# Kernel tuning notes

Hardware: AMD Instinct MI355X
Metric: run time of the kernel (lower is better)

Reference implementation:

```python
import jax, jax.numpy as jnp
import numpy as np

N, E, T, D, A = 16384, 65536, 2048, 64, 6


def _w(k, shape, fan_in):
    return jax.random.normal(k, shape, jnp.float32) / np.sqrt(fan_in)


def setup_inputs() -> dict:
    key = jax.random.key(0)
    ks = jax.random.split(key, 20)
    inp = {}
    inp["x"] = jax.random.normal(ks[0], (N, 3), jnp.float32)
    inp["edge_attr"] = jax.random.normal(ks[1], (E, 7), jnp.float32)
    inp["edge_index"] = jax.random.randint(ks[2], (2, E), 0, N)
    inp["nonring"] = jax.random.randint(ks[3], (T, 4), 0, N)
    inp["hx"] = jnp.zeros((1, D), jnp.float32)
    inp["cx"] = jnp.zeros((1, D), jnp.float32)
    inp["W_lin0"] = _w(ks[4], (D, 3), 3); inp["b_lin0"] = jnp.zeros((D,), jnp.float32)
    inp["W_e1"] = _w(ks[5], (128, 7), 7); inp["b_e1"] = jnp.zeros((128,), jnp.float32)
    inp["W_e2"] = _w(ks[6], (D * D, 128), 128); inp["b_e2"] = jnp.zeros((D * D,), jnp.float32)
    inp["conv_root"] = _w(ks[7], (D, D), D); inp["conv_bias"] = jnp.zeros((D,), jnp.float32)
    inp["gru_Wih"] = _w(ks[8], (3 * D, D), D); inp["gru_Whh"] = _w(ks[9], (3 * D, D), D)
    inp["gru_bih"] = jnp.zeros((3 * D,), jnp.float32); inp["gru_bhh"] = jnp.zeros((3 * D,), jnp.float32)
    inp["s2s_Wih"] = _w(ks[10], (4 * D, 2 * D), 2 * D); inp["s2s_Whh"] = _w(ks[11], (4 * D, D), D)
    inp["s2s_bih"] = jnp.zeros((4 * D,), jnp.float32); inp["s2s_bhh"] = jnp.zeros((4 * D,), jnp.float32)
    inp["mem_Wih"] = _w(ks[12], (4 * D, 2 * D), 2 * D); inp["mem_Whh"] = _w(ks[13], (4 * D, D), D)
    inp["mem_bih"] = jnp.zeros((4 * D,), jnp.float32); inp["mem_bhh"] = jnp.zeros((4 * D,), jnp.float32)
    inp["W_lin1"] = _w(ks[14], (D, 5 * D), 5 * D); inp["b_lin1"] = jnp.zeros((D,), jnp.float32)
    inp["W_lin2"] = _w(ks[15], (A, D), D); inp["b_lin2"] = jnp.zeros((A,), jnp.float32)
    inp["W_lin3"] = _w(ks[16], (1, 3 * D), 3 * D); inp["b_lin3"] = jnp.zeros((1,), jnp.float32)
    return inp


def _lstm_cell(xin, h, c, Wih, Whh, bih, bhh):
    g = xin @ Wih.T + bih + h @ Whh.T + bhh
    i, f, gg, o = jnp.split(g, 4, axis=-1)  # torch gate order i,f,g,o
    c = jax.nn.sigmoid(f) * c + jax.nn.sigmoid(i) * jnp.tanh(gg)
    h = jax.nn.sigmoid(o) * jnp.tanh(c)
    return h, c


def _gru_cell(xin, h, Wih, Whh, bih, bhh):
    gi = xin @ Wih.T + bih
    gh = h @ Whh.T + bhh
    ir, iz, inn = jnp.split(gi, 3, axis=-1)  # torch gate order r,z,n
    hr, hz, hn = jnp.split(gh, 3, axis=-1)
    r = jax.nn.sigmoid(ir + hr)
    z = jax.nn.sigmoid(iz + hz)
    n = jnp.tanh(inn + r * hn)
    return (1.0 - z) * n + z * h


def reference(x, edge_attr, edge_index, nonring, hx, cx,
              W_lin0, b_lin0, W_e1, b_e1, W_e2, b_e2, conv_root, conv_bias,
              gru_Wih, gru_Whh, gru_bih, gru_bhh,
              s2s_Wih, s2s_Whh, s2s_bih, s2s_bhh,
              mem_Wih, mem_Whh, mem_bih, mem_bhh,
              W_lin1, b_lin1, W_lin2, b_lin2, W_lin3, b_lin3):
    src, tgt = edge_index[0], edge_index[1]
    out = jax.nn.relu(x @ W_lin0.T + b_lin0)  # [N, D]
    h = out  # GRU hidden (nodes as batch)
    # edge-conditioned dim x dim matrices (NNConv edge MLP)
    ew = jax.nn.relu(edge_attr @ W_e1.T + b_e1)
    ew = (ew @ W_e2.T + b_e2).reshape(E, D, D)  # [E, D, D]
    cnt = jnp.maximum(jax.ops.segment_sum(jnp.ones((E,), out.dtype), tgt, num_segments=N), 1.0)
    for _ in range(3):
        msg = jnp.einsum('ed,edf->ef', out[src], ew)  # per-edge small matmul
        aggr = jax.ops.segment_sum(msg, tgt, num_segments=N) / cnt[:, None]  # scatter-mean
        m = jax.nn.relu(aggr + out @ conv_root + conv_bias)  # NNConv root + bias, then relu
        h = _gru_cell(m, h, gru_Wih, gru_Whh, gru_bih, gru_bhh)
        out = h
    # Set2Set pooling (single graph, B=1), processing_steps=3
    hs = jnp.zeros((1, D), out.dtype)
    cs = jnp.zeros((1, D), out.dtype)
    q_star = jnp.zeros((1, 2 * D), out.dtype)
    for _ in range(3):
        hs, cs = _lstm_cell(q_star, hs, cs, s2s_Wih, s2s_Whh, s2s_bih, s2s_bhh)
        a = jax.nn.softmax(out @ hs[0])  # [N]
        r = (a[:, None] * out).sum(0, keepdims=True)  # [1, D]
        q_star = jnp.concatenate([hs, r], axis=1)
    pool = q_star  # [1, 2D]
    lstm_out, cx_new = _lstm_cell(pool, hx, cx, mem_Wih, mem_Whh, mem_bih, mem_bhh)
    hx_new = lstm_out
    # torsion head: index_select -> view(4*D, -1) -> permute(1,0)
    sel = out[nonring.reshape(-1)]  # [4T, D]
    tfeat = sel.reshape(4 * D, -1).T  # [T, 4D], faithful to torch view semantics
    rep = jnp.repeat(lstm_out.reshape(-1), T).reshape(T, D)  # torch repeat_interleave + view
    pf = jnp.concatenate([tfeat, rep], axis=1)  # [T, 5D]
    logits = jax.nn.relu(pf @ W_lin1.T + b_lin1) @ W_lin2.T + b_lin2  # [T, A]
    v = jnp.concatenate([pool, lstm_out], axis=1) @ W_lin3.T + b_lin3  # [1, 1]
    return logits, v, hx_new, cx_new
```

## Files before the change

### kernel.cpp

```cpp
#include <hip/hip_runtime.h>

#define cN 16384
#define cE 65536
#define cT 2048
#define CAP 88

typedef __attribute__((ext_vector_type(8))) short short8;
typedef __attribute__((ext_vector_type(4))) float f32x4;
typedef __attribute__((ext_vector_type(4))) unsigned u32x4;

__device__ __forceinline__ short f2bf(float f){
  unsigned u = __float_as_uint(f);
  u = (u + 0x7FFFu + ((u >> 16) & 1u)) >> 16;
  return (short)u;
}
__device__ __forceinline__ float bf2f(short s){
  return __uint_as_float(((unsigned)(unsigned short)s) << 16);
}
__device__ __forceinline__ unsigned cvtpk(float lo, float hi){
  unsigned r;
  asm("v_cvt_pk_bf16_f32 %0, %1, %2" : "=v"(r) : "v"(lo), "v"(hi));
  return r;
}
__device__ __forceinline__ float sigm(float x){ return 1.f / (1.f + __expf(-x)); }
__device__ __forceinline__ float wred(float v){
  v += __shfl_xor(v, 32); v += __shfl_xor(v, 16); v += __shfl_xor(v, 8);
  v += __shfl_xor(v, 4);  v += __shfl_xor(v, 2);  v += __shfl_xor(v, 1);
  return v;
}
__device__ __forceinline__ float wredmax(float v){
  v = fmaxf(v, __shfl_xor(v, 32)); v = fmaxf(v, __shfl_xor(v, 16));
  v = fmaxf(v, __shfl_xor(v, 8));  v = fmaxf(v, __shfl_xor(v, 4));
  v = fmaxf(v, __shfl_xor(v, 2));  v = fmaxf(v, __shfl_xor(v, 1));
  return v;
}

#define B_L0   4096
#define B_H1   20480
#define B_W2   22528
#define B_B2   22544
#define B_WP   22656
#define B_DEG  22912
__global__ __launch_bounds__(256) void k_setup(
    const float* __restrict__ x, const float* __restrict__ Wl0, const float* __restrict__ bl0,
    float* __restrict__ out,
    const float* __restrict__ ea, const float* __restrict__ We1, const float* __restrict__ be1,
    unsigned* __restrict__ h1p,
    const float* __restrict__ W2, short* __restrict__ w2f,
    const float* __restrict__ b2, short* __restrict__ b2f,
    const float* __restrict__ convW, const float* __restrict__ gWih,
    const float* __restrict__ gWhh, short* __restrict__ wpk,
    const int* __restrict__ ei, int* __restrict__ deg)
{
  int b = blockIdx.x, tid = threadIdx.x;
  if (b < B_L0){
    int i = b * 256 + tid;
    int n = i >> 6, f = i & 63;
    float acc = bl0[f] + x[n*3]*Wl0[f*3] + x[n*3+1]*Wl0[f*3+1] + x[n*3+2]*Wl0[f*3+2];
    out[i] = fmaxf(acc, 0.f);
  } else if (b < B_H1){
    int i = (b - B_L0) * 256 + tid;
    int e = i >> 6, k = i & 63;
    const float* a  = ea + e * 7;
    const float* w0 = We1 + k * 7;
    const float* w1 = We1 + (k + 64) * 7;
    float a0 = be1[k], a1 = be1[k + 64];
    #pragma unroll
    for (int c = 0; c < 7; c++){ float av = a[c]; a0 += av * w0[c]; a1 += av * w1[c]; }
    unsigned lo = (unsigned short)f2bf(fmaxf(a0, 0.f));
    unsigned hi = (unsigned short)f2bf(fmaxf(a1, 0.f));
    h1p[i] = lo | (hi << 16);
  } else if (b < B_W2){
    int o = (b - B_H1) * 256 + tid;
    int j = o & 7, l = (o >> 3) & 63, ks = (o >> 9) & 31, c = (o >> 14) & 7, fb = (o >> 17) & 3;
    int f = fb * 16 + (l & 15);
    int d = c * 8 + j;
    int k = ks * 4 + ((l >> 4) & 3);
    w2f[o] = f2bf(W2[(d * 64 + f) * 128 + k]);
  } else if (b < B_B2){
    int o = (b - B_W2) * 256 + tid;
    int j = o & 7, l = (o >> 3) & 63, ks2 = (o >> 9) & 1, fb = (o >> 10) & 3;
    int d = ks2 * 32 + ((l >> 4) & 3) * 8 + j;
    int f = fb * 16 + (l & 15);
    b2f[o] = f2bf(b2[d * 64 + f]);
  } else if (b < B_WP){
    int o = (b - B_B2) * 256 + tid;
    int j = o & 7, l = (o >> 3) & 63, kc = (o >> 9) & 1, cb = o >> 10;
    int k = kc * 32 + ((l >> 4) & 3) * 8 + j;
    int c16 = l & 15;
    float v;
    if (cb < 4)       v = convW[k * 64 + cb * 16 + c16];
    else if (cb < 16) v = gWih[((cb - 4) * 16 + c16) * 64 + k];
    else              v = gWhh[((cb - 16) * 16 + c16) * 64 + k];
    wpk[o] = f2bf(v);
  } else {
    int e = (b - B_WP) * 256 + tid;
    atomicAdd(&deg[ei[cE + e]], 1);
  }
}

__global__ __launch_bounds__(1024) void k_scan(const int* __restrict__ deg,
    int* __restrict__ rowp, int* __restrict__ cur, float* __restrict__ cnt)
{
  __shared__ int part[1024];
  int tid = threadIdx.x;
  int base = tid * 16;
  int loc[16]; int s = 0;
  #pragma unroll
  for (int i = 0; i < 16; i++){ loc[i] = s; s += deg[base + i]; }
  part[tid] = s;
  __syncthreads();
  for (int off = 1; off < 1024; off <<= 1){
    int v = (tid >= off) ? part[tid - off] : 0;
    __syncthreads();
    part[tid] += v;
    __syncthreads();
  }
  int inc = part[tid];
  int eb = inc - s;
  #pragma unroll
  for (int i = 0; i < 16; i++){
    int rv = eb + loc[i];
    rowp[base + i] = rv;
    cur[base + i] = rv;
    int dv = deg[base + i];
    cnt[base + i] = (float)(dv > 0 ? dv : 1);
  }
  if (tid == 1023) rowp[16384] = inc;
}

__global__ __launch_bounds__(256) void k_scatter(const int* __restrict__ ei,
    int* __restrict__ cur, int* __restrict__ esrc, int* __restrict__ eidx)
{
  int e = blockIdx.x * 256 + threadIdx.x;
  int t = ei[cE + e];
  int pos = atomicAdd(&cur[t], 1);
  esrc[pos] = ei[e];
  eidx[pos] = e;
}

__global__ __launch_bounds__(256) void k_sagg(const float* __restrict__ outR,
    float* __restrict__ outW,
    const unsigned* __restrict__ h1p, const short* __restrict__ w2f,
    const short* __restrict__ b2f, const short* __restrict__ wpk,
    const float* __restrict__ convB, const float* __restrict__ bih,
    const float* __restrict__ bhh, const float* __restrict__ cnt,
    const int* __restrict__ rowp, const int* __restrict__ esrc,
    const int* __restrict__ eidx)
{
  __shared__ __align__(16) short S[16][1040];
  __shared__ __align__(16) unsigned h1i[CAP][64];
  __shared__ __align__(16) float outsf[CAP][64];
  __shared__ __align__(16) short osb[16][72];
  __shared__ int ordb[32];
  int tid = threadIdx.x, w = tid >> 6, lane = tid & 63;
  int t0 = blockIdx.x * 16;

  int ebase = rowp[t0];
  int eend  = rowp[t0 + 16];
  int ecnt  = eend - ebase;
  bool fits = (ecnt <= CAP);
  int scnt  = fits ? ecnt : CAP;
  for (int i = w; i < scnt; i += 4){
    int eid = eidx[ebase + i];
    int src = esrc[ebase + i];
    h1i[i][lane] = h1p[(size_t)eid * 64 + lane];
    outsf[i][lane] = outR[(size_t)src * 64 + lane];
  }
  if (tid < 16) ordb[tid] = rowp[t0 + tid + 1] - rowp[t0 + tid];
  __syncthreads();
  if (tid < 16){
    int d = ordb[tid];
    int rank = 0;
    #pragma unroll
    for (int j = 0; j < 16; j++){
      int dj = ordb[j];
      rank += (dj > d) || (dj == d && j < tid);
    }
    ordb[16 + rank] = tid;
  }
  __syncthreads();
  int tsel[4], toff[4], tcnt[4];
  #pragma unroll
  for (int g = 0; g < 4; g++){
    int pos = g * 4 + ((g & 1) ? (3 - w) : w);
    int ti = ordb[16 + pos];
    tsel[g] = ti;
    int t = t0 + ti;
    int a = rowp[t], b = rowp[t + 1];
    toff[g] = a - ebase; tcnt[g] = b - a;
  }

  #pragma unroll
  for (int g = 0; g < 4; g++){
    int ti = tsel[g];
    float os = 0.f;
    int tf = toff[g], tc = tcnt[g];
    for (int p = 0; p < tc; p++){
      int slot = tf + p;
      if (slot < CAP) os += outsf[slot][lane];
      else            os += outR[(size_t)esrc[ebase + slot] * 64 + lane];
    }
    osb[ti][lane] = (short)cvtpk(os, os);
  }

  f32x4 acc[4] = {{0,0,0,0},{0,0,0,0},{0,0,0,0},{0,0,0,0}};
  int arow = lane & 15, kg = lane >> 4;
  for (int c = 0; c < 8; ++c){
    #pragma unroll
    for (int g = 0; g < 4; ++g){
      int ti = tsel[g];
      float a0[8], a1[8];
      #pragma unroll
      for (int d = 0; d < 8; d++){ a0[d] = 0.f; a1[d] = 0.f; }
      int tc = tcnt[g], tf = toff[g];
      if (fits){
        #pragma unroll 2
        for (int p = 0; p < tc; ++p){
          int slot = tf + p;
          unsigned u = h1i[slot][lane];
          float h1a = __uint_as_float(u << 16);
          float h1b = __uint_as_float(u & 0xFFFF0000u);
          f32x4 o0 = *(const f32x4*)&outsf[slot][c * 8];
          f32x4 o1 = *(const f32x4*)&outsf[slot][c * 8 + 4];
          a0[0] = fmaf(o0[0], h1a, a0[0]); a1[0] = fmaf(o0[0], h1b, a1[0]);
          a0[1] = fmaf(o0[1], h1a, a0[1]); a1[1] = fmaf(o0[1], h1b, a1[1]);
          a0[2] = fmaf(o0[2], h1a, a0[2]); a1[2] = fmaf(o0[2], h1b, a1[2]);
          a0[3] = fmaf(o0[3], h1a, a0[3]); a1[3] = fmaf(o0[3], h1b, a1[3]);
          a0[4] = fmaf(o1[0], h1a, a0[4]); a1[4] = fmaf(o1[0], h1b, a1[4]);
          a0[5] = fmaf(o1[1], h1a, a0[5]); a1[5] = fmaf(o1[1], h1b, a1[5]);
          a0[6] = fmaf(o1[2], h1a, a0[6]); a1[6] = fmaf(o1[2], h1b, a1[6]);
          a0[7] = fmaf(o1[3], h1a, a0[7]); a1[7] = fmaf(o1[3], h1b, a1[7]);
        }
      } else {
        for (int p = 0; p < tc; ++p){
          int slot = tf + p;
          if (slot < CAP){
            unsigned u = h1i[slot][lane];
            float h1a = __uint_as_float(u << 16);
            float h1b = __uint_as_float(u & 0xFFFF0000u);
            f32x4 o0 = *(const f32x4*)&outsf[slot][c * 8];
            f32x4 o1 = *(const f32x4*)&outsf[slot][c * 8 + 4];
            #pragma unroll
            for (int d = 0; d < 4; d++){
              a0[d] = fmaf(o0[d], h1a, a0[d]); a1[d] = fmaf(o0[d], h1b, a1[d]);
              a0[4+d] = fmaf(o1[d], h1a, a0[4+d]); a1[4+d] = fmaf(o1[d], h1b, a1[4+d]);
            }
          } else {
            int eid = eidx[ebase + slot];
            int src = esrc[ebase + slot];
            unsigned u = h1p[(size_t)eid * 64 + lane];
            float h1a = __uint_as_float(u << 16);
            float h1b = __uint_as_float(u & 0xFFFF0000u);
            #pragma unroll
            for (int d = 0; d < 8; d++){
              float o = outR[(size_t)src * 64 + c * 8 + d];
              a0[d] = fmaf(o, h1a, a0[d]); a1[d] = fmaf(o, h1b, a1[d]);
            }
          }
        }
      }
      u32x4 p0, p1;
      p0[0] = cvtpk(a0[0], a0[1]); p0[1] = cvtpk(a0[2], a0[3]);
      p0[2] = cvtpk(a0[4], a0[5]); p0[3] = cvtpk(a0[6], a0[7]);
      p1[0] = cvtpk(a1[0], a1[1]); p1[1] = cvtpk(a1[2], a1[3]);
      p1[2] = cvtpk(a1[4], a1[5]); p1[3] = cvtpk(a1[6], a1[7]);
      *(u32x4*)&S[ti][lane * 8]       = p0;
      *(u32x4*)&S[ti][512 + lane * 8] = p1;
    }
    __syncthreads();
    const short* bbase = w2f + ((size_t)(w * 8 + c) * 32) * 512 + lane * 8;
    #pragma unroll
    for (int ks8 = 0; ks8 < 8; ++ks8){
      #pragma unroll
      for (int j = 0; j < 4; ++j){
        int ks = ks8 * 4 + j;
        short8 afr = *(const short8*)&S[arow][ks * 32 + kg * 8];
        short8 bfr = *(const short8*)(bbase + (size_t)ks * 512);
        acc[j] = __builtin_amdgcn_mfma_f32_16x16x32_bf16(afr, bfr, acc[j], 0, 0, 0);
      }
    }
    __syncthreads();
  }
  #pragma unroll
  for (int ks2 = 0; ks2 < 2; ++ks2){
    short8 osf = *(const short8*)&osb[arow][ks2 * 32 + kg * 8];
    short8 bfr = *(const short8*)(b2f + ((size_t)((w * 2 + ks2) * 64 + lane)) * 8);
    acc[ks2] = __builtin_amdgcn_mfma_f32_16x16x32_bf16(osf, bfr, acc[ks2], 0, 0, 0);
  }
  f32x4 accT;
  #pragma unroll
  for (int q = 0; q < 4; q++)
    accT[q] = (acc[0][q] + acc[1][q]) + (acc[2][q] + acc[3][q]);

  int fcol = w * 16 + arow;
  int trow = kg * 4;
  short* tA  = (short*)&h1i[0][0];
  short* mAp = tA + 16 * 72;
  for (int i = tid; i < 512; i += 256){
    int r = i >> 5, c2 = (i & 31) * 2;
    float2 v = *(const float2*)&outR[(size_t)(t0 + r) * 64 + c2];
    *(unsigned*)&tA[r * 72 + c2] = cvtpk(v.x, v.y);
  }
  __syncthreads();
  const short8* WF = (const short8*)wpk;
  short8 aof0 = *(const short8*)&tA[arow * 72 + kg * 8];
  short8 aof1 = *(const short8*)&tA[arow * 72 + 32 + kg * 8];
  f32x4 cz = {0.f, 0.f, 0.f, 0.f};
  f32x4 cva0 = __builtin_amdgcn_mfma_f32_16x16x32_bf16(aof0, WF[(w * 2 + 0) * 64 + lane], cz, 0, 0, 0);
  f32x4 cva1 = __builtin_amdgcn_mfma_f32_16x16x32_bf16(aof1, WF[(w * 2 + 1) * 64 + lane], cz, 0, 0, 0);
  float cb_ = convB[fcol];
  #pragma unroll
  for (int q = 0; q < 4; q++){
    int node = t0 + trow + q;
    float icq = 1.0f / fmaxf(cnt[node], 1.0f);
    float m = fmaxf(accT[q] * icq + cva0[q] + cva1[q] + cb_, 0.f);
    mAp[(trow + q) * 72 + fcol] = f2bf(m);
  }
  __syncthreads();
  short8 amf0 = *(const short8*)&mAp[arow * 72 + kg * 8];
  short8 amf1 = *(const short8*)&mAp[arow * 72 + 32 + kg * 8];
  f32x4 gir = {0,0,0,0}, giz = {0,0,0,0}, gin = {0,0,0,0};
  f32x4 ghr = {0,0,0,0}, ghz = {0,0,0,0}, ghn = {0,0,0,0};
  gir = __builtin_amdgcn_mfma_f32_16x16x32_bf16(amf0, WF[((4  + w) * 2 + 0) * 64 + lane], gir, 0, 0, 0);
  gir = __builtin_amdgcn_mfma_f32_16x16x32_bf16(amf1, WF[((4  + w) * 2 + 1) * 64 + lane], gir, 0, 0, 0);
  giz = __builtin_amdgcn_mfma_f32_16x16x32_bf16(amf0, WF[((8  + w) * 2 + 0) * 64 + lane], giz, 0, 0, 0);
  giz = __builtin_amdgcn_mfma_f32_16x16x32_bf16(amf1, WF[((8  + w) * 2 + 1) * 64 + lane], giz, 0, 0, 0);
  gin = __builtin_amdgcn_mfma_f32_16x16x32_bf16(amf0, WF[((12 + w) * 2 + 0) * 64 + lane], gin, 0, 0, 0);
  gin = __builtin_amdgcn_mfma_f32_16x16x32_bf16(amf1, WF[((12 + w) * 2 + 1) * 64 + lane], gin, 0, 0, 0);
  ghr = __builtin_amdgcn_mfma_f32_16x16x32_bf16(aof0, WF[((16 + w) * 2 + 0) * 64 + lane], ghr, 0, 0, 0);
  ghr = __builtin_amdgcn_mfma_f32_16x16x32_bf16(aof1, WF[((16 + w) * 2 + 1) * 64 + lane], ghr, 0, 0, 0);
  ghz = __builtin_amdgcn_mfma_f32_16x16x32_bf16(aof0, WF[((20 + w) * 2 + 0) * 64 + lane], ghz, 0, 0, 0);
  ghz = __builtin_amdgcn_mfma_f32_16x16x32_bf16(aof1, WF[((20 + w) * 2 + 1) * 64 + lane], ghz, 0, 0, 0);
  ghn = __builtin_amdgcn_mfma_f32_16x16x32_bf16(aof0, WF[((24 + w) * 2 + 0) * 64 + lane], ghn, 0, 0, 0);
  ghn = __builtin_amdgcn_mfma_f32_16x16x32_bf16(aof1, WF[((24 + w) * 2 + 1) * 64 + lane], ghn, 0, 0, 0);
  float bir = bih[fcol], biz = bih[64 + fcol], bin_ = bih[128 + fcol];
  float bhr = bhh[fcol], bhz = bhh[64 + fcol], bhn = bhh[128 + fcol];
  #pragma unroll
  for (int q = 0; q < 4; q++){
    size_t node = (size_t)(t0 + trow + q);
    float rr = sigm(gir[q] + bir + ghr[q] + bhr);
    float zz = sigm(giz[q] + biz + ghz[q] + bhz);
    float nn = tanhf(gin[q] + bin_ + rr * (ghn[q] + bhn));
    float o = outR[node * 64 + fcol];
    outW[node * 64 + fcol] = (1.f - zz) * nn + zz * o;
  }
}

__global__ __launch_bounds__(256) void k_dotsF(const float* __restrict__ out,
    const float* __restrict__ Wih, const float* __restrict__ Whh,
    const float* __restrict__ bih, const float* __restrict__ bhh,
    float* __restrict__ scal,
    const float* __restrict__ rbI, const float* __restrict__ bmI, const float* __restrict__ esI,
    float* __restrict__ rbO, float* __restrict__ bmO, float* __restrict__ esO, int st)
{
  __shared__ float q[128];
  __shared__ float hsL[64];
  __shared__ float gsh[4][64];
  __shared__ float hsh[64];
  __shared__ float smax[4];
  __shared__ float otile[64][64];
  __shared__ float sarr[64];
  __shared__ float ebuf[64];
  __shared__ float rpart[4][64];
  __shared__ float redA[4], redB[4];
  const float* pg = scal + st * 256;
  float* pn = scal + (st + 1) * 256;
  int tid = threadIdx.x, gg = tid >> 6, lane = tid & 63;
  if (st > 0){
    float bm = bmI[tid];
    float m = wredmax(bm);
    if (lane == 0) redA[gg] = m;
    __syncthreads();
    float gmax = fmaxf(fmaxf(redA[0], redA[1]), fmaxf(redA[2], redA[3]));
    float ep = wred(__expf(bm - gmax) * esI[tid]);
    if (lane == 0) redB[gg] = ep;
    float racc = 0.f;
    for (int i = 0; i < 64; i++){
      int b = gg * 64 + i;
      racc += __expf(bmI[b] - gmax) * rbI[b * 64 + lane];
    }
    rpart[gg][lane] = racc;
    __syncthreads();
    if (gg == 0){
      float esum = redB[0] + redB[1] + redB[2] + redB[3];
      float r = rpart[0][lane] + rpart[1][lane] + rpart[2][lane] + rpart[3][lane];
      q[64 + lane] = r / esum;
    }
  } else if (gg == 0) q[64 + lane] = 0.f;
  if (gg == 0){
    float hs = (st == 0) ? 0.f : pg[lane];
    q[lane] = hs; hsL[lane] = hs;
  }
  __syncthreads();
  float2 fq = *(const float2*)&q[2 * lane];
  float hv0 = hsL[lane];
  #pragma unroll 4
  for (int o = 0; o < 64; o++){
    int row = gg * 64 + o;
    float2 wv = *(const float2*)&Wih[(size_t)row * 128 + 2 * lane];
    float s = wv.x * fq.x + wv.y * fq.y + Whh[(size_t)row * 64 + lane] * hv0;
    s = wred(s);
    if (lane == 0) gsh[gg][o] = s;
  }
  __syncthreads();
  if (gg == 0){
    float gi = gsh[0][lane] + bih[lane]       + bhh[lane];
    float gf = gsh[1][lane] + bih[64 + lane]  + bhh[64 + lane];
    float gv = gsh[2][lane] + bih[128 + lane] + bhh[128 + lane];
    float go = gsh[3][lane] + bih[192 + lane] + bhh[192 + lane];
    float cs = (st == 0) ? 0.f : pg[64 + lane];
    float cn = sigm(gf) * cs + sigm(gi) * tanhf(gv);
    float hn = sigm(go) * tanhf(cn);
    hsh[lane] = hn;
    if (blockIdx.x == 0){ pn[lane] = hn; pn[64 + lane] = cn; }
  }
  __syncthreads();
  int nbase = blockIdx.x * 64 + gg * 16;
  float hv = hsh[lane];
  float wmax = -3.4e38f;
  #pragma unroll 4
  for (int i = 0; i < 16; i++){
    float v = out[(size_t)(nbase + i) * 64 + lane];
    otile[gg * 16 + i][lane] = v;
    float p = wred(v * hv);
    if (lane == 0) sarr[gg * 16 + i] = p;
    wmax = fmaxf(wmax, p);
  }
  if (lane == 0) smax[gg] = wmax;
  __syncthreads();
  float bm = fmaxf(fmaxf(smax[0], smax[1]), fmaxf(smax[2], smax[3]));
  if (tid < 64) ebuf[tid] = __expf(sarr[tid] - bm);
  __syncthreads();
  float racc = 0.f;
  #pragma unroll 4
  for (int i = 0; i < 16; i++)
    racc += ebuf[gg * 16 + i] * otile[gg * 16 + i][lane];
  rpart[gg][lane] = racc;
  __syncthreads();
  if (gg == 0){
    float r = rpart[0][lane] + rpart[1][lane] + rpart[2][lane] + rpart[3][lane];
    rbO[blockIdx.x * 64 + lane] = r;
  } else if (gg == 1){
    float es = wred(ebuf[lane]);
    if (lane == 0) esO[blockIdx.x] = es;
  } else if (gg == 2 && lane == 0) bmO[blockIdx.x] = bm;
}

__global__ __launch_bounds__(256) void k_smFin(
    const float* __restrict__ rbI, const float* __restrict__ bmI, const float* __restrict__ esI,
    const float* __restrict__ Wih, const float* __restrict__ Whh,
    const float* __restrict__ bih, const float* __restrict__ bhh,
    const float* __restrict__ hx, const float* __restrict__ cx,
    const float* __restrict__ W3, const float* __restrict__ b3,
    float* __restrict__ scal, float* __restrict__ dout)
{
  __shared__ float redA[4], redB[4];
  __shared__ float rpart[4][64];
  __shared__ float pool[128];
  __shared__ float hxs[64];
  __shared__ float gsh[4][64];
  __shared__ float lob[64];
  int tid = threadIdx.x, wid = tid >> 6, lane = tid & 63;
  float bm = bmI[tid];
  float m = wredmax(bm);
  if (lane == 0) redA[wid] = m;
  __syncthreads();
  float gmax = fmaxf(fmaxf(redA[0], redA[1]), fmaxf(redA[2], redA[3]));
  float ep = wred(__expf(bm - gmax) * esI[tid]);
  if (lane == 0) redB[wid] = ep;
  float racc = 0.f;
  for (int i = 0; i < 64; i++){
    int b = wid * 64 + i;
    racc += __expf(bmI[b] - gmax) * rbI[b * 64 + lane];
  }
  rpart[wid][lane] = racc;
  __syncthreads();
  if (wid == 0){
    float esum = redB[0] + redB[1] + redB[2] + redB[3];
    float r = rpart[0][lane] + rpart[1][lane] + rpart[2][lane] + rpart[3][lane];
    pool[lane] = scal[3 * 256 + lane];
    pool[64 + lane] = r / esum;
    hxs[lane] = hx[lane];
  }
  __syncthreads();
  float2 fq = *(const float2*)&pool[2 * lane];
  float hv = hxs[lane];
  #pragma unroll 4
  for (int o = 0; o < 64; o++){
    int row = wid * 64 + o;
    float2 wv = *(const float2*)&Wih[(size_t)row * 128 + 2 * lane];
    float s = wv.x * fq.x + wv.y * fq.y + Whh[(size_t)row * 64 + lane] * hv;
    s = wred(s);
    if (lane == 0) gsh[wid][o] = s;
  }
  __syncthreads();
  if (wid == 0){
    float gi = gsh[0][lane] + bih[lane]       + bhh[lane];
    float gf = gsh[1][lane] + bih[64 + lane]  + bhh[64 + lane];
    float gv = gsh[2][lane] + bih[128 + lane] + bhh[128 + lane];
    float go = gsh[3][lane] + bih[192 + lane] + bhh[192 + lane];
    float cn = sigm(gf) * cx[lane] + sigm(gi) * tanhf(gv);
    float hn = sigm(go) * tanhf(cn);
    dout[12289 + lane] = hn;
    dout[12353 + lane] = cn;
    scal[1024 + lane] = hn;
    lob[lane] = hn;
  }
  __syncthreads();
  if (wid == 0){
    float a = pool[lane] * W3[lane] + pool[64 + lane] * W3[64 + lane]
            + lob[lane] * W3[128 + lane];
    a = wred(a);
    if (lane == 0) dout[12288] = a + b3[0];
  }
}

__global__ __launch_bounds__(256) void k_head(const float* __restrict__ out,
    const int* __restrict__ nr, const float* __restrict__ scal,
    const float* __restrict__ W1, const float* __restrict__ b1,
    const float* __restrict__ W2, const float* __restrict__ b2,
    float* __restrict__ dout)
{
  __shared__ float pf[4][320];
  __shared__ float hb[4][64];
  int tid = threadIdx.x, wid = tid >> 6, lane = tid & 63;
  int t = blockIdx.x * 4 + wid;
  float lo = scal[1024 + (t >> 5)];
  #pragma unroll
  for (int rep = 0; rep < 4; rep++){
    int j = rep * 64 + lane;
    int idx = nr[j * 32 + (t >> 6)];
    pf[wid][j] = out[idx * 64 + (t & 63)];
  }
  pf[wid][256 + lane] = lo;
  __syncthreads();
  float acc = b1[lane];
  const float* w = W1 + lane * 320;
  #pragma unroll 4
  for (int j = 0; j < 320; j++) acc += pf[wid][j] * w[j];
  hb[wid][lane] = fmaxf(acc, 0.f);
  __syncthreads();
  if (lane < 6){
    float a2 = b2[lane];
    const float* w2 = W2 + lane * 64;
    #pragma unroll 4
    for (int f = 0; f < 64; f++) a2 += hb[wid][f] * w2[f];
    dout[t * 6 + lane] = a2;
  }
}

extern "C" void kernel_launch(void* const* d_in, const int* in_sizes, int n_in,
                              void* d_out, int out_size, void* d_ws, size_t ws_size,
                              hipStream_t stream)
{
  const float* x         = (const float*)d_in[0];
  const float* edge_attr = (const float*)d_in[1];
  const int*   ei        = (const int*)d_in[2];
  const int*   nonring   = (const int*)d_in[3];
  const float* hx        = (const float*)d_in[4];
  const float* cx        = (const float*)d_in[5];
  const float* W_lin0 = (const float*)d_in[6];  const float* b_lin0 = (const float*)d_in[7];
  const float* W_e1   = (const float*)d_in[8];  const float* b_e1   = (const float*)d_in[9];
  const float* W_e2   = (const float*)d_in[10]; const float* b_e2   = (const float*)d_in[11];
  const float* convW  = (const float*)d_in[12]; const float* convB  = (const float*)d_in[13];
  const float* gWih   = (const float*)d_in[14]; const float* gWhh   = (const float*)d_in[15];
  const float* gbih   = (const float*)d_in[16]; const float* gbhh   = (const float*)d_in[17];
  const float* sWih   = (const float*)d_in[18]; const float* sWhh   = (const float*)d_in[19];
  const float* sbih   = (const float*)d_in[20]; const float* sbhh   = (const float*)d_in[21];
  const float* mWih   = (const float*)d_in[22]; const float* mWhh   = (const float*)d_in[23];
  const float* mbih   = (const float*)d_in[24]; const float* mbhh   = (const float*)d_in[25];
  const float* W_lin1 = (const float*)d_in[26]; const float* b_lin1 = (const float*)d_in[27];
  const float* W_lin2 = (const float*)d_in[28]; const float* b_lin2 = (const float*)d_in[29];
  const float* W_lin3 = (const float*)d_in[30]; const float* b_lin3 = (const float*)d_in[31];
  float* dout = (float*)d_out;

  char* w = (char*)d_ws;
  float* outb = (float*)w;  w += (size_t)cN * 64 * 4;
  float* outb2= (float*)w;  w += (size_t)cN * 64 * 4;
  unsigned* h1p = (unsigned*)w;  w += (size_t)cE * 64 * 4;
  short* w2f  = (short*)w;  w += (size_t)64 * 8192 * 2;
  short* b2f  = (short*)w;  w += 4096 * 2;
  short* wpk  = (short*)w;  w += 28672 * 2;
  float* cntb = (float*)w;  w += cN * 4;
  float* rbufA= (float*)w;  w += 256 * 64 * 4;
  float* rbufB= (float*)w;  w += 256 * 64 * 4;
  float* bmA  = (float*)w;  w += 256 * 4;
  float* bmB  = (float*)w;  w += 256 * 4;
  float* esA  = (float*)w;  w += 256 * 4;
  float* esB  = (float*)w;  w += 256 * 4;
  float* scal = (float*)w;  w += 1088 * 4;
  int* deg  = (int*)w;  w += cN * 4;
  int* cur  = (int*)w;  w += cN * 4;
  int* rowp = (int*)w;  w += (cN + 1) * 4 + 60;
  int* esrc = (int*)w;  w += cE * 4;
  int* eidx = (int*)w;  w += cE * 4;

  hipMemsetAsync(deg, 0, cN * 4, stream);

  k_setup<<<B_DEG, 256, 0, stream>>>(x, W_lin0, b_lin0, outb,
      edge_attr, W_e1, b_e1, h1p, W_e2, w2f, b_e2, b2f,
      convW, gWih, gWhh, wpk, ei, deg);
  k_scan<<<1, 1024, 0, stream>>>(deg, rowp, cur, cntb);
  k_scatter<<<cE / 256, 256, 0, stream>>>(ei, cur, esrc, eidx);

  k_sagg<<<cN / 16, 256, 0, stream>>>(outb,  outb2, h1p, w2f, b2f, wpk, convB,
      gbih, gbhh, cntb, rowp, esrc, eidx);
  k_sagg<<<cN / 16, 256, 0, stream>>>(outb2, outb,  h1p, w2f, b2f, wpk, convB,
      gbih, gbhh, cntb, rowp, esrc, eidx);
  k_sagg<<<cN / 16, 256, 0, stream>>>(outb,  outb2, h1p, w2f, b2f, wpk, convB,
      gbih, gbhh, cntb, rowp, esrc, eidx);

  k_dotsF<<<cN / 64, 256, 0, stream>>>(outb2, sWih, sWhh, sbih, sbhh, scal,
      rbufA, bmA, esA, rbufA, bmA, esA, 0);
  k_dotsF<<<cN / 64, 256, 0, stream>>>(outb2, sWih, sWhh, sbih, sbhh, scal,
      rbufA, bmA, esA, rbufB, bmB, esB, 1);
  k_dotsF<<<cN / 64, 256, 0, stream>>>(outb2, sWih, sWhh, sbih, sbhh, scal,
      rbufB, bmB, esB, rbufA, bmA, esA, 2);
  k_smFin<<<1, 256, 0, stream>>>(rbufA, bmA, esA,
      mWih, mWhh, mbih, mbhh, hx, cx, W_lin3, b_lin3, scal, dout);

  k_head<<<cT / 4, 256, 0, stream>>>(outb2, nonring, scal, W_lin1, b_lin1, W_lin2, b_lin2, dout);
}
```

Baseline: 484.0 us.

## Warp-specialize sagg into producer and MFMA consumer waves with double buffering

Doubles the block to 512 threads and splits it by role. Waves 0-3 build the per-edge outer-product tile S for chunk c. Waves 4-7 run the MFMA contraction on chunk c-1 from the other half of a double-buffered S. The aim is to overlap the VALU FMA aggregation with the matrix-core work, which were previously serialized behind two barriers per chunk. The cost is a larger LDS footprint and a block size that may cut residency, and only half the waves do the final GRU epilogue.

```diff
diff --git a/kernel.cpp b/kernel.cpp
--- a/kernel.cpp
+++ b/kernel.cpp
@@ -139,7 +139,7 @@
   eidx[pos] = e;
 }
 
-__global__ __launch_bounds__(256) void k_sagg(const float* __restrict__ outR,
+__global__ __launch_bounds__(512) void k_sagg(const float* __restrict__ outR,
     float* __restrict__ outW,
     const unsigned* __restrict__ h1p, const short* __restrict__ w2f,
     const short* __restrict__ b2f, const short* __restrict__ wpk,
@@ -148,12 +148,14 @@
     const int* __restrict__ rowp, const int* __restrict__ esrc,
     const int* __restrict__ eidx)
 {
-  __shared__ __align__(16) short S[16][1040];
+  __shared__ __align__(16) short S[2][16][1040];
   __shared__ __align__(16) unsigned h1i[CAP][64];
   __shared__ __align__(16) float outsf[CAP][64];
   __shared__ __align__(16) short osb[16][72];
   __shared__ int ordb[32];
   int tid = threadIdx.x, w = tid >> 6, lane = tid & 63;
+  bool prod = (w < 4);
+  int pw = w & 3;
   int t0 = blockIdx.x * 16;
 
   int ebase = rowp[t0];
@@ -161,7 +163,7 @@
   int ecnt  = eend - ebase;
   bool fits = (ecnt <= CAP);
   int scnt  = fits ? ecnt : CAP;
-  for (int i = w; i < scnt; i += 4){
+  for (int i = w; i < scnt; i += 8){
     int eid = eidx[ebase + i];
     int src = esrc[ebase + i];
     h1i[i][lane] = h1p[(size_t)eid * 64 + lane];
@@ -180,170 +182,187 @@
     ordb[16 + rank] = tid;
   }
   __syncthreads();
+
   int tsel[4], toff[4], tcnt[4];
-  #pragma unroll
-  for (int g = 0; g < 4; g++){
-    int pos = g * 4 + ((g & 1) ? (3 - w) : w);
-    int ti = ordb[16 + pos];
-    tsel[g] = ti;
-    int t = t0 + ti;
-    int a = rowp[t], b = rowp[t + 1];
-    toff[g] = a - ebase; tcnt[g] = b - a;
-  }
-
-  #pragma unroll
-  for (int g = 0; g < 4; g++){
-    int ti = tsel[g];
-    float os = 0.f;
-    int tf = toff[g], tc = tcnt[g];
-    for (int p = 0; p < tc; p++){
-      int slot = tf + p;
-      if (slot < CAP) os += outsf[slot][lane];
-      else            os += outR[(size_t)esrc[ebase + slot] * 64 + lane];
-    }
-    osb[ti][lane] = (short)cvtpk(os, os);
+  if (prod){
+    #pragma unroll
+    for (int g = 0; g < 4; g++){
+      int pos = g * 4 + ((g & 1) ? (3 - pw) : pw);
+      int ti = ordb[16 + pos];
+      tsel[g] = ti;
+      int t = t0 + ti;
+      int a = rowp[t], b = rowp[t + 1];
+      toff[g] = a - ebase; tcnt[g] = b - a;
+    }
+    #pragma unroll
+    for (int g = 0; g < 4; g++){
+      int ti = tsel[g];
+      float os = 0.f;
+      int tf = toff[g], tc = tcnt[g];
+      for (int p = 0; p < tc; p++){
+        int slot = tf + p;
+        if (slot < CAP) os += outsf[slot][lane];
+        else            os += outR[(size_t)esrc[ebase + slot] * 64 + lane];
+      }
+      osb[ti][lane] = (short)cvtpk(os, os);
+    }
   }
 
   f32x4 acc[4] = {{0,0,0,0},{0,0,0,0},{0,0,0,0},{0,0,0,0}};
   int arow = lane & 15, kg = lane >> 4;
-  for (int c = 0; c < 8; ++c){
-    #pragma unroll
-    for (int g = 0; g < 4; ++g){
-      int ti = tsel[g];
-      float a0[8], a1[8];
-      #pragma unroll
-      for (int d = 0; d < 8; d++){ a0[d] = 0.f; a1[d] = 0.f; }
-      int tc = tcnt[g], tf = toff[g];
-      if (fits){
-        #pragma unroll 2
-        for (int p = 0; p < tc; ++p){
-          int slot = tf + p;
-          unsigned u = h1i[slot][lane];
-          float h1a = __uint_as_float(u << 16);
-          float h1b = __uint_as_float(u & 0xFFFF0000u);
-          f32x4 o0 = *(const f32x4*)&outsf[slot][c * 8];
-          f32x4 o1 = *(const f32x4*)&outsf[slot][c * 8 + 4];
-          a0[0] = fmaf(o0[0], h1a, a0[0]); a1[0] = fmaf(o0[0], h1b, a1[0]);
-          a0[1] = fmaf(o0[1], h1a, a0[1]); a1[1] = fmaf(o0[1], h1b, a1[1]);
-          a0[2] = fmaf(o0[2], h1a, a0[2]); a1[2] = fmaf(o0[2], h1b, a1[2]);
-          a0[3] = fmaf(o0[3], h1a, a0[3]); a1[3] = fmaf(o0[3], h1b, a1[3]);
-          a0[4] = fmaf(o1[0], h1a, a0[4]); a1[4] = fmaf(o1[0], h1b, a1[4]);
-          a0[5] = fmaf(o1[1], h1a, a0[5]); a1[5] = fmaf(o1[1], h1b, a1[5]);
-          a0[6] = fmaf(o1[2], h1a, a0[6]); a1[6] = fmaf(o1[2], h1b, a1[6]);
-          a0[7] = fmaf(o1[3], h1a, a0[7]); a1[7] = fmaf(o1[3], h1b, a1[7]);
+  short* tA  = (short*)&h1i[0][0];
+  short* mAp = tA + 16 * 72;
+
+  for (int ph = 0; ph <= 8; ++ph){
+    if (prod){
+      if (ph < 8){
+        int c = ph;
+        int buf = c & 1;
+        #pragma unroll
+        for (int g = 0; g < 4; ++g){
+          int ti = tsel[g];
+          float a0[8], a1[8];
+          #pragma unroll
+          for (int d = 0; d < 8; d++){ a0[d] = 0.f; a1[d] = 0.f; }
+          int tc = tcnt[g], tf = toff[g];
+          if (fits){
+            #pragma unroll 2
+            for (int p = 0; p < tc; ++p){
+              int slot = tf + p;
+              unsigned u = h1i[slot][lane];
+              float h1a = __uint_as_float(u << 16);
+              float h1b = __uint_as_float(u & 0xFFFF0000u);
+              f32x4 o0 = *(const f32x4*)&outsf[slot][c * 8];
+              f32x4 o1 = *(const f32x4*)&outsf[slot][c * 8 + 4];
+              a0[0] = fmaf(o0[0], h1a, a0[0]); a1[0] = fmaf(o0[0], h1b, a1[0]);
+              a0[1] = fmaf(o0[1], h1a, a0[1]); a1[1] = fmaf(o0[1], h1b, a1[1]);
+              a0[2] = fmaf(o0[2], h1a, a0[2]); a1[2] = fmaf(o0[2], h1b, a1[2]);
+              a0[3] = fmaf(o0[3], h1a, a0[3]); a1[3] = fmaf(o0[3], h1b, a1[3]);
+              a0[4] = fmaf(o1[0], h1a, a0[4]); a1[4] = fmaf(o1[0], h1b, a1[4]);
+              a0[5] = fmaf(o1[1], h1a, a0[5]); a1[5] = fmaf(o1[1], h1b, a1[5]);
+              a0[6] = fmaf(o1[2], h1a, a0[6]); a1[6] = fmaf(o1[2], h1b, a1[6]);
+              a0[7] = fmaf(o1[3], h1a, a0[7]); a1[7] = fmaf(o1[3], h1b, a1[7]);
+            }
+          } else {
+            for (int p = 0; p < tc; ++p){
+              int slot = tf + p;
+              if (slot < CAP){
+                unsigned u = h1i[slot][lane];
+                float h1a = __uint_as_float(u << 16);
+                float h1b = __uint_as_float(u & 0xFFFF0000u);
+                f32x4 o0 = *(const f32x4*)&outsf[slot][c * 8];
+                f32x4 o1 = *(const f32x4*)&outsf[slot][c * 8 + 4];
+                #pragma unroll
+                for (int d = 0; d < 4; d++){
+                  a0[d] = fmaf(o0[d], h1a, a0[d]); a1[d] = fmaf(o0[d], h1b, a1[d]);
+                  a0[4+d] = fmaf(o1[d], h1a, a0[4+d]); a1[4+d] = fmaf(o1[d], h1b, a1[4+d]);
+                }
+              } else {
+                int eid = eidx[ebase + slot];
+                int src = esrc[ebase + slot];
+                unsigned u = h1p[(size_t)eid * 64 + lane];
+                float h1a = __uint_as_float(u << 16);
+                float h1b = __uint_as_float(u & 0xFFFF0000u);
+                #pragma unroll
+                for (int d = 0; d < 8; d++){
+                  float o = outR[(size_t)src * 64 + c * 8 + d];
+                  a0[d] = fmaf(o, h1a, a0[d]); a1[d] = fmaf(o, h1b, a1[d]);
+                }
+              }
+            }
+          }
+          u32x4 p0, p1;
+          p0[0] = cvtpk(a0[0], a0[1]); p0[1] = cvtpk(a0[2], a0[3]);
+          p0[2] = cvtpk(a0[4], a0[5]); p0[3] = cvtpk(a0[6], a0[7]);
+          p1[0] = cvtpk(a1[0], a1[1]); p1[1] = cvtpk(a1[2], a1[3]);
+          p1[2] = cvtpk(a1[4], a1[5]); p1[3] = cvtpk(a1[6], a1[7]);
+          *(u32x4*)&S[buf][ti][lane * 8]       = p0;
+          *(u32x4*)&S[buf][ti][512 + lane * 8] = p1;
         }
       } else {
-        for (int p = 0; p < tc; ++p){
-          int slot = tf + p;
-          if (slot < CAP){
-            unsigned u = h1i[slot][lane];
-            float h1a = __uint_as_float(u << 16);
-            float h1b = __uint_as_float(u & 0xFFFF0000u);
-            f32x4 o0 = *(const f32x4*)&outsf[slot][c * 8];
-            f32x4 o1 = *(const f32x4*)&outsf[slot][c * 8 + 4];
-            #pragma unroll
-            for (int d = 0; d < 4; d++){
-              a0[d] = fmaf(o0[d], h1a, a0[d]); a1[d] = fmaf(o0[d], h1b, a1[d]);
-              a0[4+d] = fmaf(o1[d], h1a, a0[4+d]); a1[4+d] = fmaf(o1[d], h1b, a1[4+d]);
-            }
-          } else {
-            int eid = eidx[ebase + slot];
-            int src = esrc[ebase + slot];
-            unsigned u = h1p[(size_t)eid * 64 + lane];
-            float h1a = __uint_as_float(u << 16);
-            float h1b = __uint_as_float(u & 0xFFFF0000u);
-            #pragma unroll
-            for (int d = 0; d < 8; d++){
-              float o = outR[(size_t)src * 64 + c * 8 + d];
-              a0[d] = fmaf(o, h1a, a0[d]); a1[d] = fmaf(o, h1b, a1[d]);
-            }
-          }
+        for (int i = tid; i < 512; i += 256){
+          int r = i >> 5, c2 = (i & 31) * 2;
+          float2 v = *(const float2*)&outR[(size_t)(t0 + r) * 64 + c2];
+          *(unsigned*)&tA[r * 72 + c2] = cvtpk(v.x, v.y);
         }
       }
-      u32x4 p0, p1;
-      p0[0] = cvtpk(a0[0], a0[1]); p0[1] = cvtpk(a0[2], a0[3]);
-      p0[2] = cvtpk(a0[4], a0[5]); p0[3] = cvtpk(a0[6], a0[7]);
-      p1[0] = cvtpk(a1[0], a1[1]); p1[1] = cvtpk(a1[2], a1[3]);
-      p1[2] = cvtpk(a1[4], a1[5]); p1[3] = cvtpk(a1[6], a1[7]);
-      *(u32x4*)&S[ti][lane * 8]       = p0;
-      *(u32x4*)&S[ti][512 + lane * 8] = p1;
+    } else if (ph > 0){
+      int c = ph - 1;
+      int buf = c & 1;
+      const short* bbase = w2f + ((size_t)(pw * 8 + c) * 32) * 512 + lane * 8;
+      #pragma unroll
+      for (int ks8 = 0; ks8 < 8; ++ks8){
+        #pragma unroll
+        for (int j = 0; j < 4; ++j){
+          int ks = ks8 * 4 + j;
+          short8 afr = *(const short8*)&S[buf][arow][ks * 32 + kg * 8];
+          short8 bfr = *(const short8*)(bbase + (size_t)ks * 512);
+          acc[j] = __builtin_amdgcn_mfma_f32_16x16x32_bf16(afr, bfr, acc[j], 0, 0, 0);
+        }
+      }
     }
     __syncthreads();
-    const short* bbase = w2f + ((size_t)(w * 8 + c) * 32) * 512 + lane * 8;
-    #pragma unroll
-    for (int ks8 = 0; ks8 < 8; ++ks8){
-      #pragma unroll
-      for (int j = 0; j < 4; ++j){
-        int ks = ks8 * 4 + j;
-        short8 afr = *(const short8*)&S[arow][ks * 32 + kg * 8];
-        short8 bfr = *(const short8*)(bbase + (size_t)ks * 512);
-        acc[j] = __builtin_amdgcn_mfma_f32_16x16x32_bf16(afr, bfr, acc[j], 0, 0, 0);
-      }
-    }
-    __syncthreads();
-  }
-  #pragma unroll
-  for (int ks2 = 0; ks2 < 2; ++ks2){
-    short8 osf = *(const short8*)&osb[arow][ks2 * 32 + kg * 8];
-    short8 bfr = *(const short8*)(b2f + ((size_t)((w * 2 + ks2) * 64 + lane)) * 8);
-    acc[ks2] = __builtin_amdgcn_mfma_f32_16x16x32_bf16(osf, bfr, acc[ks2], 0, 0, 0);
-  }
-  f32x4 accT;
-  #pragma unroll
-  for (int q = 0; q < 4; q++)
-    accT[q] = (acc[0][q] + acc[1][q]) + (acc[2][q] + acc[3][q]);
-
-  int fcol = w * 16 + arow;
+  }
+
+  const short8* WF = (const short8*)wpk;
+  int fcol = pw * 16 + arow;
   int trow = kg * 4;
-  short* tA  = (short*)&h1i[0][0];
-  short* mAp = tA + 16 * 72;
-  for (int i = tid; i < 512; i += 256){
-    int r = i >> 5, c2 = (i & 31) * 2;
-    float2 v = *(const float2*)&outR[(size_t)(t0 + r) * 64 + c2];
-    *(unsigned*)&tA[r * 72 + c2] = cvtpk(v.x, v.y);
-  }
-  __syncthreads();
-  const short8* WF = (const short8*)wpk;
-  short8 aof0 = *(const short8*)&tA[arow * 72 + kg * 8];
-  short8 aof1 = *(const short8*)&tA[arow * 72 + 32 + kg * 8];
-  f32x4 cz = {0.f, 0.f, 0.f, 0.f};
-  f32x4 cva0 = __builtin_amdgcn_mfma_f32_16x16x32_bf16(aof0, WF[(w * 2 + 0) * 64 + lane], cz, 0, 0, 0);
-  f32x4 cva1 = __builtin_amdgcn_mfma_f32_16x16x32_bf16(aof1, WF[(w * 2 + 1) * 64 + lane], cz, 0, 0, 0);
-  float cb_ = convB[fcol];
-  #pragma unroll
-  for (int q = 0; q < 4; q++){
-    int node = t0 + trow + q;
-    float icq = 1.0f / fmaxf(cnt[node], 1.0f);
-    float m = fmaxf(accT[q] * icq + cva0[q] + cva1[q] + cb_, 0.f);
-    mAp[(trow + q) * 72 + fcol] = f2bf(m);
-  }
-  __syncthreads();
-  short8 amf0 = *(const short8*)&mAp[arow * 72 + kg * 8];
-  short8 amf1 = *(const short8*)&mAp[arow * 72 + 32 + kg * 8];
-  f32x4 gir = {0,0,0,0}, giz = {0,0,0,0}, gin = {0,0,0,0};
-  f32x4 ghr = {0,0,0,0}, ghz = {0,0,0,0}, ghn = {0,0,0,0};
-  gir = __builtin_amdgcn_mfma_f32_16x16x32_bf16(amf0, WF[((4  + w) * 2 + 0) * 64 + lane], gir, 0, 0, 0);
-  gir = __builtin_amdgcn_mfma_f32_16x16x32_bf16(amf1, WF[((4  + w) * 2 + 1) * 64 + lane], gir, 0, 0, 0);
-  giz = __builtin_amdgcn_mfma_f32_16x16x32_bf16(amf0, WF[((8  + w) * 2 + 0) * 64 + lane], giz, 0, 0, 0);
-  giz = __builtin_amdgcn_mfma_f32_16x16x32_bf16(amf1, WF[((8  + w) * 2 + 1) * 64 + lane], giz, 0, 0, 0);
-  gin = __builtin_amdgcn_mfma_f32_16x16x32_bf16(amf0, WF[((12 + w) * 2 + 0) * 64 + lane], gin, 0, 0, 0);
-  gin = __builtin_amdgcn_mfma_f32_16x16x32_bf16(amf1, WF[((12 + w) * 2 + 1) * 64 + lane], gin, 0, 0, 0);
-  ghr = __builtin_amdgcn_mfma_f32_16x16x32_bf16(aof0, WF[((16 + w) * 2 + 0) * 64 + lane], ghr, 0, 0, 0);
-  ghr = __builtin_amdgcn_mfma_f32_16x16x32_bf16(aof1, WF[((16 + w) * 2 + 1) * 64 + lane], ghr, 0, 0, 0);
-  ghz = __builtin_amdgcn_mfma_f32_16x16x32_bf16(aof0, WF[((20 + w) * 2 + 0) * 64 + lane], ghz, 0, 0, 0);
-  ghz = __builtin_amdgcn_mfma_f32_16x16x32_bf16(aof1, WF[((20 + w) * 2 + 1) * 64 + lane], ghz, 0, 0, 0);
-  ghn = __builtin_amdgcn_mfma_f32_16x16x32_bf16(aof0, WF[((24 + w) * 2 + 0) * 64 + lane], ghn, 0, 0, 0);
-  ghn = __builtin_amdgcn_mfma_f32_16x16x32_bf16(aof1, WF[((24 + w) * 2 + 1) * 64 + lane], ghn, 0, 0, 0);
-  float bir = bih[fcol], biz = bih[64 + fcol], bin_ = bih[128 + fcol];
-  float bhr = bhh[fcol], bhz = bhh[64 + fcol], bhn = bhh[128 + fcol];
-  #pragma unroll
-  for (int q = 0; q < 4; q++){
-    size_t node = (size_t)(t0 + trow + q);
-    float rr = sigm(gir[q] + bir + ghr[q] + bhr);
-    float zz = sigm(giz[q] + biz + ghz[q] + bhz);
-    float nn = tanhf(gin[q] + bin_ + rr * (ghn[q] + bhn));
-    float o = outR[node * 64 + fcol];
-    outW[node * 64 + fcol] = (1.f - zz) * nn + zz * o;
+  if (!prod){
+    #pragma unroll
+    for (int ks2 = 0; ks2 < 2; ++ks2){
+      short8 osf = *(const short8*)&osb[arow][ks2 * 32 + kg * 8];
+      short8 bfr = *(const short8*)(b2f + ((size_t)((pw * 2 + ks2) * 64 + lane)) * 8);
+      acc[ks2] = __builtin_amdgcn_mfma_f32_16x16x32_bf16(osf, bfr, acc[ks2], 0, 0, 0);
+    }
+    f32x4 accT;
+    #pragma unroll
+    for (int q = 0; q < 4; q++)
+      accT[q] = (acc[0][q] + acc[1][q]) + (acc[2][q] + acc[3][q]);
+    short8 aof0 = *(const short8*)&tA[arow * 72 + kg * 8];
+    short8 aof1 = *(const short8*)&tA[arow * 72 + 32 + kg * 8];
+    f32x4 cz = {0.f, 0.f, 0.f, 0.f};
+    f32x4 cva0 = __builtin_amdgcn_mfma_f32_16x16x32_bf16(aof0, WF[(pw * 2 + 0) * 64 + lane], cz, 0, 0, 0);
+    f32x4 cva1 = __builtin_amdgcn_mfma_f32_16x16x32_bf16(aof1, WF[(pw * 2 + 1) * 64 + lane], cz, 0, 0, 0);
+    float cb_ = convB[fcol];
+    #pragma unroll
+    for (int q = 0; q < 4; q++){
+      int node = t0 + trow + q;
+      float icq = 1.0f / fmaxf(cnt[node], 1.0f);
+      float m = fmaxf(accT[q] * icq + cva0[q] + cva1[q] + cb_, 0.f);
+      mAp[(trow + q) * 72 + fcol] = f2bf(m);
+    }
+  }
+  __syncthreads();
+  if (!prod){
+    short8 aof0 = *(const short8*)&tA[arow * 72 + kg * 8];
+    short8 aof1 = *(const short8*)&tA[arow * 72 + 32 + kg * 8];
+    short8 amf0 = *(const short8*)&mAp[arow * 72 + kg * 8];
+    short8 amf1 = *(const short8*)&mAp[arow * 72 + 32 + kg * 8];
+    f32x4 gir = {0,0,0,0}, giz = {0,0,0,0}, gin = {0,0,0,0};
+    f32x4 ghr = {0,0,0,0}, ghz = {0,0,0,0}, ghn = {0,0,0,0};
+    gir = __builtin_amdgcn_mfma_f32_16x16x32_bf16(amf0, WF[((4  + pw) * 2 + 0) * 64 + lane], gir, 0, 0, 0);
+    gir = __builtin_amdgcn_mfma_f32_16x16x32_bf16(amf1, WF[((4  + pw) * 2 + 1) * 64 + lane], gir, 0, 0, 0);
+    giz = __builtin_amdgcn_mfma_f32_16x16x32_bf16(amf0, WF[((8  + pw) * 2 + 0) * 64 + lane], giz, 0, 0, 0);
+    giz = __builtin_amdgcn_mfma_f32_16x16x32_bf16(amf1, WF[((8  + pw) * 2 + 1) * 64 + lane], giz, 0, 0, 0);
+    gin = __builtin_amdgcn_mfma_f32_16x16x32_bf16(amf0, WF[((12 + pw) * 2 + 0) * 64 + lane], gin, 0, 0, 0);
+    gin = __builtin_amdgcn_mfma_f32_16x16x32_bf16(amf1, WF[((12 + pw) * 2 + 1) * 64 + lane], gin, 0, 0, 0);
+    ghr = __builtin_amdgcn_mfma_f32_16x16x32_bf16(aof0, WF[((16 + pw) * 2 + 0) * 64 + lane], ghr, 0, 0, 0);
+    ghr = __builtin_amdgcn_mfma_f32_16x16x32_bf16(aof1, WF[((16 + pw) * 2 + 1) * 64 + lane], ghr, 0, 0, 0);
+    ghz = __builtin_amdgcn_mfma_f32_16x16x32_bf16(aof0, WF[((20 + pw) * 2 + 0) * 64 + lane], ghz, 0, 0, 0);
+    ghz = __builtin_amdgcn_mfma_f32_16x16x32_bf16(aof1, WF[((20 + pw) * 2 + 1) * 64 + lane], ghz, 0, 0, 0);
+    ghn = __builtin_amdgcn_mfma_f32_16x16x32_bf16(aof0, WF[((24 + pw) * 2 + 0) * 64 + lane], ghn, 0, 0, 0);
+    ghn = __builtin_amdgcn_mfma_f32_16x16x32_bf16(aof1, WF[((24 + pw) * 2 + 1) * 64 + lane], ghn, 0, 0, 0);
+    float bir = bih[fcol], biz = bih[64 + fcol], bin_ = bih[128 + fcol];
+    float bhr = bhh[fcol], bhz = bhh[64 + fcol], bhn = bhh[128 + fcol];
+    #pragma unroll
+    for (int q = 0; q < 4; q++){
+      size_t node = (size_t)(t0 + trow + q);
+      float rr = sigm(gir[q] + bir + ghr[q] + bhr);
+      float zz = sigm(giz[q] + biz + ghz[q] + bhz);
+      float nn = tanhf(gin[q] + bin_ + rr * (ghn[q] + bhn));
+      float o = outR[node * 64 + fcol];
+      outW[node * 64 + fcol] = (1.f - zz) * nn + zz * o;
+    }
   }
 }
 
@@ -604,11 +623,11 @@
   k_scan<<<1, 1024, 0, stream>>>(deg, rowp, cur, cntb);
   k_scatter<<<cE / 256, 256, 0, stream>>>(ei, cur, esrc, eidx);
 
-  k_sagg<<<cN / 16, 256, 0, stream>>>(outb,  outb2, h1p, w2f, b2f, wpk, convB,
+  k_sagg<<<cN / 16, 512, 0, stream>>>(outb,  outb2, h1p, w2f, b2f, wpk, convB,
       gbih, gbhh, cntb, rowp, esrc, eidx);
-  k_sagg<<<cN / 16, 256, 0, stream>>>(outb2, outb,  h1p, w2f, b2f, wpk, convB,
+  k_sagg<<<cN / 16, 512, 0, stream>>>(outb2, outb,  h1p, w2f, b2f, wpk, convB,
       gbih, gbhh, cntb, rowp, esrc, eidx);
-  k_sagg<<<cN / 16, 256, 0, stream>>>(outb,  outb2, h1p, w2f, b2f, wpk, convB,
+  k_sagg<<<cN / 16, 512, 0, stream>>>(outb,  outb2, h1p, w2f, b2f, wpk, convB,
       gbih, gbhh, cntb, rowp, esrc, eidx);
 
   k_dotsF<<<cN / 64, 256, 0, stream>>>(outb2, sWih, sWhh, sbih, sbhh, scal,
```

After: 557.1 us. 1.15x slower.
